# Kernel optimization log

Measured on AMD Instinct MI355X. Metric: run time of the kernel, lower is better.

Reference implementation:

```python
import jax, jax.numpy as jnp
import numpy as np

B, D, H, E, K, A = 65536, 44, 256, 4, 2, 8  # batch, state_dim, hidden, experts, top_k, action_dim


def setup_inputs() -> dict:
    key = jax.random.key(0)
    ks = jax.random.split(key, 10)
    s = 0.1  # weight scale
    return dict(
        state=jax.random.normal(ks[0], (B, D), dtype=jnp.float32),
        rW1=jax.random.normal(ks[1], (D, H // 2)) * s, rb1=jnp.zeros((H // 2,)),
        rW2=jax.random.normal(ks[2], (H // 2, E)) * s, rb2=jnp.zeros((E,)),
        eW1=jax.random.normal(ks[3], (E, D, H)) * s, eb1=jnp.zeros((E, H)),
        eg1=jnp.ones((E, H)), ebt1=jnp.zeros((E, H)),
        eW2=jax.random.normal(ks[4], (E, H, H)) * s, eb2=jnp.zeros((E, H)),
        eg2=jnp.ones((E, H)), ebt2=jnp.zeros((E, H)),
        eW3=jax.random.normal(ks[5], (E, H, 2 * A)) * s, eb3=jnp.zeros((E, 2 * A)),
        vW1=jax.random.normal(ks[6], (D, H)) * s, vb1=jnp.zeros((H,)),
        vg=jnp.ones((H,)), vbt=jnp.zeros((H,)),
        vW2=jax.random.normal(ks[7], (H, H // 2)) * s, vb2=jnp.zeros((H // 2,)),
        vW3=jax.random.normal(ks[8], (H // 2, 1)) * s, vb3=jnp.zeros((1,)),
    )


def _ln(x, g, b):
    m = jnp.mean(x, axis=-1, keepdims=True)
    v = jnp.mean(jnp.square(x - m), axis=-1, keepdims=True)
    return (x - m) * jax.lax.rsqrt(v + 1e-5) * g + b


def reference(state, rW1, rb1, rW2, rb2,
              eW1, eb1, eg1, ebt1, eW2, eb2, eg2, ebt2, eW3, eb3,
              vW1, vb1, vg, vbt, vW2, vb2, vW3, vb3):
    # Router (eval mode: no noise)
    h = jax.nn.relu(state @ rW1 + rb1)
    router_probs = jax.nn.softmax(h @ rW2 + rb2, axis=-1)          # [B, E]
    top_v, top_i = jax.lax.top_k(router_probs, K)                  # [B, K]
    top_v = top_v / (jnp.sum(top_v, axis=-1, keepdims=True) + 1e-8)
    # Dense combine weights per expert (equivalent to per-sample gather/scatter loop)
    combine = jnp.sum(jax.nn.one_hot(top_i, E, dtype=state.dtype) * top_v[..., None], axis=1)  # [B, E]

    def expert(W1, b1, g1, bt1, W2, b2, g2, bt2, W3, b3):
        y = jax.nn.relu(_ln(state @ W1 + b1, g1, bt1))   # [B, H]
        y = jax.nn.relu(_ln(y @ W2 + b2, g2, bt2))       # [B, H]
        return y @ W3 + b3                               # [B, 2A]

    eout = jax.vmap(expert)(eW1, eb1, eg1, ebt1, eW2, eb2, eg2, ebt2, eW3, eb3)  # [E, B, 2A]
    mix = jnp.einsum('ebd,be->bd', eout, combine)        # [B, 2A]

    alpha = jax.nn.softplus(mix[:, :A]) + 1.0
    beta = jax.nn.softplus(mix[:, A:]) + 1.0

    v = jax.nn.relu(_ln(state @ vW1 + vb1, vg, vbt))
    v = jax.nn.relu(v @ vW2 + vb2)
    value = v @ vW3 + vb3                                # [B, 1]
    return alpha, beta, value, router_probs
```

## Files before the change

kernel.cpp:

```cpp
#include <hip/hip_runtime.h>
#include <math.h>

#define NB 65536

using f32x4 = __attribute__((ext_vector_type(4))) float;
using u32x4 = __attribute__((ext_vector_type(4))) unsigned;
using bf16x8 = __attribute__((ext_vector_type(8))) __bf16;

__device__ __forceinline__ unsigned pk2(float lo, float hi) {
    return (unsigned)__builtin_bit_cast(unsigned short, (__bf16)lo)
         | ((unsigned)__builtin_bit_cast(unsigned short, (__bf16)hi) << 16);
}
__device__ __forceinline__ float softplus_f(float x) {
    return fmaxf(x, 0.f) + log1pf(expf(-fabsf(x)));
}

#define MFMA16(acc, a, b) acc = __builtin_amdgcn_mfma_f32_16x16x32_bf16(a, b, acc, 0, 0, 0)

__device__ __forceinline__ bf16x8 cvt8(f32x4 a, f32x4 b) {
    union { bf16x8 v; unsigned u[4]; } r;
    r.u[0] = pk2(a[0], a[1]); r.u[1] = pk2(a[2], a[3]);
    r.u[2] = pk2(b[0], b[1]); r.u[3] = pk2(b[2], b[3]);
    return r.v;
}

__device__ __forceinline__ const bf16x8* ys_frag(const unsigned short* ys, int row, int col) {
    return (const bf16x8*)&ys[row * 256 + (col ^ ((row & 7) << 3))];
}

template<int NJ>
__device__ __forceinline__ void ldch(f32x4* r, const f32x4* __restrict__ src, int tid) {
    #pragma unroll
    for (int j = 0; j < NJ; ++j) r[j] = src[tid + j * 256];
}
template<int NJ>
__device__ __forceinline__ void wrch(unsigned short* buf, const f32x4* r, int tid) {
    #pragma unroll
    for (int j = 0; j < NJ; ++j) *(f32x4*)&buf[(size_t)(tid + j * 256) * 8] = r[j];
}

template<int NT>
__device__ __forceinline__ void mfma_bcols(f32x4* acc, bf16x8 a, const unsigned short* bufp, int c, int g) {
    #pragma unroll
    for (int t = 0; t < NT; ++t) {
        bf16x8 b = *(const bf16x8*)&bufp[t * 512 + g * 128 + c * 8];
        MFMA16(acc[t], a, b);
    }
}

__device__ __forceinline__ void ln_relu_store(
    f32x4* acc, const float* bs, const float* gs, const float* ts,
    unsigned int* ysu, int stripe, int g, int c)
{
    #pragma unroll
    for (int t = 0; t < 16; ++t) {
        float bb = bs[t * 16 + c];
        #pragma unroll
        for (int r = 0; r < 4; ++r) acc[t][r] += bb;
    }
    float sum[4] = {0.f, 0.f, 0.f, 0.f}, sq[4] = {0.f, 0.f, 0.f, 0.f};
    #pragma unroll
    for (int t = 0; t < 16; ++t) {
        #pragma unroll
        for (int r = 0; r < 4; ++r) { sum[r] += acc[t][r]; sq[r] += acc[t][r] * acc[t][r]; }
    }
    #pragma unroll
    for (int m = 1; m < 16; m <<= 1) {
        #pragma unroll
        for (int r = 0; r < 4; ++r) { sum[r] += __shfl_xor(sum[r], m); sq[r] += __shfl_xor(sq[r], m); }
    }
    float rs[4], nm[4];
    #pragma unroll
    for (int r = 0; r < 4; ++r) {
        float mean = sum[r] * (1.f / 256.f);
        float var = sq[r] * (1.f / 256.f) - mean * mean;
        rs[r] = rsqrtf(var + 1e-5f);
        nm[r] = -mean * rs[r];
    }
    const int odd = c & 1;
    const int ra = stripe + g * 4 + (odd ? 2 : 0);
    const int sza = (ra & 7) << 2, szb = ((ra + 1) & 7) << 2;
    #pragma unroll
    for (int t = 0; t < 16; ++t) {
        float gg = gs[t * 16 + c], bb = ts[t * 16 + c];
        float v0 = fmaxf(fmaf(fmaf(acc[t][0], rs[0], nm[0]), gg, bb), 0.f);
        float v1 = fmaxf(fmaf(fmaf(acc[t][1], rs[1], nm[1]), gg, bb), 0.f);
        float v2 = fmaxf(fmaf(fmaf(acc[t][2], rs[2], nm[2]), gg, bb), 0.f);
        float v3 = fmaxf(fmaf(fmaf(acc[t][3], rs[3], nm[3]), gg, bb), 0.f);
        float o0 = __shfl_xor(v0, 1), o1 = __shfl_xor(v1, 1);
        float o2 = __shfl_xor(v2, 1), o3 = __shfl_xor(v3, 1);
        unsigned p0 = pk2(odd ? o0 : v0, odd ? v0 : o0);
        unsigned p1 = pk2(odd ? o1 : v1, odd ? v1 : o1);
        unsigned p2 = pk2(odd ? o2 : v2, odd ? v2 : o2);
        unsigned p3 = pk2(odd ? o3 : v3, odd ? v3 : o3);
        unsigned pa = odd ? p2 : p0;
        unsigned pb = odd ? p3 : p1;
        int cp = t * 8 + (c >> 1);
        ysu[ra * 128 + (cp ^ sza)] = pa;
        ysu[(ra + 1) * 128 + (cp ^ szb)] = pb;
    }
}

__global__ __launch_bounds__(256) void k1_prep_router(
    const float* __restrict__ state,
    const float* __restrict__ rW1, const float* __restrict__ rb1,
    const float* __restrict__ rW2, const float* __restrict__ rb2,
    const float* __restrict__ eW1, const float* __restrict__ eW2, const float* __restrict__ eW3,
    const float* __restrict__ vW1, const float* __restrict__ vW2,
    unsigned int* __restrict__ w1img, unsigned int* __restrict__ w2img,
    unsigned int* __restrict__ vw1img, unsigned int* __restrict__ vw2img,
    unsigned int* __restrict__ w3img,
    float* __restrict__ out_probs, float* __restrict__ combine)
{
    const int blk = blockIdx.x;
    if (blk < 192) {
        int fid = blk * 256 + threadIdx.x;
        float v[8];
        unsigned int* dst;
        if (fid < 8192) {
            int e = fid >> 11, ch = (fid >> 10) & 1, rr = fid & 1023;
            int t = rr >> 6, g = (rr >> 4) & 3, c = rr & 15;
            int h = t * 16 + c, k0 = ch * 32 + g * 8;
            #pragma unroll
            for (int j = 0; j < 8; ++j) {
                int k = k0 + j;
                v[j] = (k < 44) ? eW1[(e * 44 + k) * 256 + h] : 0.f;
            }
            dst = w1img + (size_t)fid * 4;
        } else if (fid < 40960) {
            int f = fid - 8192;
            int e = f >> 13, ch = (f >> 10) & 7, rr = f & 1023;
            int t = rr >> 6, g = (rr >> 4) & 3, c = rr & 15;
            int h = t * 16 + c, k0 = ch * 32 + g * 8;
            const float* base = eW2 + (size_t)e * 65536 + h;
            #pragma unroll
            for (int j = 0; j < 8; ++j) v[j] = base[(size_t)(k0 + j) * 256];
            dst = w2img + (size_t)f * 4;
        } else if (fid < 43008) {
            int f = fid - 40960;
            int ch = f >> 10, rr = f & 1023;
            int t = rr >> 6, g = (rr >> 4) & 3, c = rr & 15;
            int h = t * 16 + c, k0 = ch * 32 + g * 8;
            #pragma unroll
            for (int j = 0; j < 8; ++j) {
                int k = k0 + j;
                v[j] = (k < 44) ? vW1[k * 256 + h] : 0.f;
            }
            dst = vw1img + (size_t)f * 4;
        } else if (fid < 47104) {
            int f = fid - 43008;
            int ch = f >> 9, rr = f & 511;
            int t = rr >> 6, g = (rr >> 4) & 3, c = rr & 15;
            int h = t * 16 + c, k0 = ch * 32 + g * 8;
            #pragma unroll
            for (int j = 0; j < 8; ++j) v[j] = vW2[(k0 + j) * 128 + h];
            dst = vw2img + (size_t)f * 4;
        } else {
            int f = fid - 47104;
            int e = f >> 9, rr = f & 511;
            int s = rr >> 6, g = (rr >> 4) & 3, o = rr & 15;
            int k0 = s * 32 + g * 8;
            #pragma unroll
            for (int j = 0; j < 8; ++j) v[j] = eW3[(size_t)e * 4096 + (k0 + j) * 16 + o];
            dst = w3img + (size_t)f * 4;
        }
        u32x4 out;
        #pragma unroll
        for (int p = 0; p < 4; ++p) out[p] = pk2(v[2 * p], v[2 * p + 1]);
        *(u32x4*)dst = out;
        return;
    }

    int b = (blk - 192) * 256 + threadIdx.x;
    float s[44];
    const float* sp = state + (size_t)b * 44;
    #pragma unroll
    for (int d = 0; d < 44; ++d) s[d] = sp[d];

    float l0 = rb2[0], l1 = rb2[1], l2 = rb2[2], l3 = rb2[3];
    for (int j4 = 0; j4 < 32; ++j4) {
        f32x4 h = *(const f32x4*)&rb1[j4 * 4];
        #pragma unroll
        for (int d = 0; d < 44; ++d) {
            f32x4 w = *(const f32x4*)&rW1[d * 128 + j4 * 4];
            h += s[d] * w;
        }
        #pragma unroll
        for (int jj = 0; jj < 4; ++jj) {
            float hv = fmaxf(h[jj], 0.f);
            f32x4 w2 = *(const f32x4*)&rW2[(j4 * 4 + jj) * 4];
            l0 += hv * w2[0]; l1 += hv * w2[1]; l2 += hv * w2[2]; l3 += hv * w2[3];
        }
    }
    float mx = fmaxf(fmaxf(l0, l1), fmaxf(l2, l3));
    float e0 = expf(l0 - mx), e1 = expf(l1 - mx), e2 = expf(l2 - mx), e3 = expf(l3 - mx);
    float inv = 1.f / (e0 + e1 + e2 + e3);
    float p0 = e0 * inv, p1 = e1 * inv, p2 = e2 * inv, p3 = e3 * inv;
    f32x4 probs = {p0, p1, p2, p3};
    *(f32x4*)&out_probs[(size_t)b * 4] = probs;

    int i1 = 0; float v1 = p0;
    if (p1 > v1) { v1 = p1; i1 = 1; }
    if (p2 > v1) { v1 = p2; i1 = 2; }
    if (p3 > v1) { v1 = p3; i1 = 3; }
    int i2 = -1; float v2 = -1.f;
    if (i1 != 0 && p0 > v2) { v2 = p0; i2 = 0; }
    if (i1 != 1 && p1 > v2) { v2 = p1; i2 = 1; }
    if (i1 != 2 && p2 > v2) { v2 = p2; i2 = 2; }
    if (i1 != 3 && p3 > v2) { v2 = p3; i2 = 3; }
    float cn = 1.f / (v1 + v2 + 1e-8f);
    float c1 = v1 * cn, c2 = v2 * cn;
    f32x4 cm;
    cm[0] = (i1 == 0) ? c1 : (i2 == 0) ? c2 : 0.f;
    cm[1] = (i1 == 1) ? c1 : (i2 == 1) ? c2 : 0.f;
    cm[2] = (i1 == 2) ? c1 : (i2 == 2) ? c2 : 0.f;
    cm[3] = (i1 == 3) ? c1 : (i2 == 3) ? c2 : 0.f;
    *(f32x4*)&combine[(size_t)b * 4] = cm;
}

#define SM_YS    0
#define SM_BUFA  32768
#define SM_BUFB  49152
#define SM_B1    65536
#define SM_G1    66560
#define SM_T1    67584
#define SM_B2    68608
#define SM_G2    69632
#define SM_T2    70656
#define SM_B3    71680
#define SM_CMB   71744
#define SM_TOTAL 72768

#define SWAPBUF() { unsigned short* _t = cur; cur = nxt; nxt = _t; }

__global__ __launch_bounds__(256, 2) void k2_experts_value(
    const float* __restrict__ state,
    const float* __restrict__ eb1, const float* __restrict__ eg1, const float* __restrict__ ebt1,
    const float* __restrict__ eb2, const float* __restrict__ eg2, const float* __restrict__ ebt2,
    const float* __restrict__ eb3,
    const float* __restrict__ vb1, const float* __restrict__ vg, const float* __restrict__ vbt,
    const float* __restrict__ vb2, const float* __restrict__ vW3, const float* __restrict__ vb3,
    const f32x4* __restrict__ w1v, const f32x4* __restrict__ w2v,
    const f32x4* __restrict__ vw1v, const f32x4* __restrict__ vw2v,
    const f32x4* __restrict__ w3v,
    const float* __restrict__ combine,
    float* __restrict__ out_alpha, float* __restrict__ out_beta, float* __restrict__ out_value)
{
    __shared__ __align__(16) unsigned char smem[SM_TOTAL];
    unsigned short* ys = (unsigned short*)(smem + SM_YS);
    unsigned int* ysu = (unsigned int*)(smem + SM_YS);
    float* b1s = (float*)(smem + SM_B1);
    float* g1s = (float*)(smem + SM_G1);
    float* t1s = (float*)(smem + SM_T1);
    float* b2s = (float*)(smem + SM_B2);
    float* g2s = (float*)(smem + SM_G2);
    float* t2s = (float*)(smem + SM_T2);
    float* b3s = (float*)(smem + SM_B3);
    float* cmbs = (float*)(smem + SM_CMB);
    unsigned short* cur = (unsigned short*)(smem + SM_BUFA);
    unsigned short* nxt = (unsigned short*)(smem + SM_BUFB);

    const int tid = threadIdx.x;
    const int wid = tid >> 6;
    const int lane = tid & 63;
    const int c = lane & 15;
    const int g = lane >> 4;
    const int stripe = wid * 16;
    const bool is_expert = (blockIdx.x < 1024);
    const int brow = (is_expert ? blockIdx.x : (blockIdx.x - 1024)) * 64;

    bf16x8 a1[2];
    {
        const float* srow = state + (size_t)(brow + stripe + c) * 44;
        f32x4 v0 = *(const f32x4*)(srow + g * 8);
        f32x4 v1 = *(const f32x4*)(srow + g * 8 + 4);
        a1[0] = cvt8(v0, v1);
        f32x4 z = {0.f, 0.f, 0.f, 0.f};
        f32x4 w0 = z, w1 = z;
        if (g == 0) { w0 = *(const f32x4*)(srow + 32); w1 = *(const f32x4*)(srow + 36); }
        else if (g == 1) { w0 = *(const f32x4*)(srow + 40); }
        a1[1] = cvt8(w0, w1);
    }

    f32x4 r[4];

    if (is_expert) {
        cmbs[tid] = combine[(size_t)brow * 4 + tid];
        float mix0 = 0.f, mix1 = 0.f, mix2 = 0.f, mix3 = 0.f;

        ldch<4>(r, w1v, tid);
        wrch<4>(cur, r, tid);
        ldch<4>(r, w1v + 1024, tid);
        __syncthreads();

        for (int e = 0; e < 4; ++e) {
            const int en = (e < 3) ? e + 1 : 3;
            float xb1 = eb1[e * 256 + tid], xg1 = eg1[e * 256 + tid], xt1 = ebt1[e * 256 + tid];
            float xb2 = eb2[e * 256 + tid], xg2 = eg2[e * 256 + tid], xt2 = ebt2[e * 256 + tid];
            b1s[tid] = xb1; g1s[tid] = xg1; t1s[tid] = xt1;
            b2s[tid] = xb2; g2s[tid] = xg2; t2s[tid] = xt2;
            if (tid < 16) b3s[tid] = eb3[e * 16 + tid];

            f32x4 acc1[16];
            #pragma unroll
            for (int t = 0; t < 16; ++t) acc1[t] = (f32x4){0.f, 0.f, 0.f, 0.f};

            wrch<4>(nxt, r, tid);
            ldch<4>(r, w2v + (size_t)(e * 8 + 0) * 1024, tid);
            mfma_bcols<16>(acc1, a1[0], cur, c, g);
            __syncthreads(); SWAPBUF();

            wrch<4>(nxt, r, tid);
            ldch<4>(r, w2v + (size_t)(e * 8 + 1) * 1024, tid);
            mfma_bcols<16>(acc1, a1[1], cur, c, g);
            ln_relu_store(acc1, b1s, g1s, t1s, ysu, stripe, g, c);
            __syncthreads(); SWAPBUF();

            f32x4 acc2[16];
            #pragma unroll
            for (int t = 0; t < 16; ++t) acc2[t] = (f32x4){0.f, 0.f, 0.f, 0.f};

            #pragma unroll
            for (int ch = 0; ch < 7; ++ch) {
                wrch<4>(nxt, r, tid);
                if (ch < 6) ldch<4>(r, w2v + (size_t)(e * 8 + ch + 2) * 1024, tid);
                else        ldch<2>(r, w3v + (size_t)e * 512, tid);
                bf16x8 a = *ys_frag(ys, stripe + c, ch * 32 + g * 8);
                mfma_bcols<16>(acc2, a, cur, c, g);
                __syncthreads(); SWAPBUF();
            }

            wrch<2>(nxt, r, tid);
            ldch<4>(r, w1v + (size_t)(en * 2) * 1024, tid);
            {
                bf16x8 a = *ys_frag(ys, stripe + c, 7 * 32 + g * 8);
                mfma_bcols<16>(acc2, a, cur, c, g);
            }
            ln_relu_store(acc2, b2s, g2s, t2s, ysu, stripe, g, c);
            __syncthreads(); SWAPBUF();

            wrch<4>(nxt, r, tid);
            ldch<4>(r, w1v + (size_t)(en * 2 + 1) * 1024, tid);
            f32x4 acc3 = (f32x4){0.f, 0.f, 0.f, 0.f};
            #pragma unroll
            for (int s = 0; s < 8; ++s) {
                bf16x8 a = *ys_frag(ys, stripe + c, s * 32 + g * 8);
                bf16x8 b = *(const bf16x8*)&cur[s * 512 + g * 128 + c * 8];
                MFMA16(acc3, a, b);
            }
            float bb3 = b3s[c];
            mix0 += cmbs[(stripe + g * 4 + 0) * 4 + e] * (acc3[0] + bb3);
            mix1 += cmbs[(stripe + g * 4 + 1) * 4 + e] * (acc3[1] + bb3);
            mix2 += cmbs[(stripe + g * 4 + 2) * 4 + e] * (acc3[2] + bb3);
            mix3 += cmbs[(stripe + g * 4 + 3) * 4 + e] * (acc3[3] + bb3);
            __syncthreads(); SWAPBUF();
        }

        int row0 = brow + stripe + g * 4;
        float sp0 = softplus_f(mix0) + 1.f;
        float sp1 = softplus_f(mix1) + 1.f;
        float sp2 = softplus_f(mix2) + 1.f;
        float sp3 = softplus_f(mix3) + 1.f;
        if (c < 8) {
            out_alpha[(size_t)(row0 + 0) * 8 + c] = sp0;
            out_alpha[(size_t)(row0 + 1) * 8 + c] = sp1;
            out_alpha[(size_t)(row0 + 2) * 8 + c] = sp2;
            out_alpha[(size_t)(row0 + 3) * 8 + c] = sp3;
        } else {
            out_beta[(size_t)(row0 + 0) * 8 + (c - 8)] = sp0;
            out_beta[(size_t)(row0 + 1) * 8 + (c - 8)] = sp1;
            out_beta[(size_t)(row0 + 2) * 8 + (c - 8)] = sp2;
            out_beta[(size_t)(row0 + 3) * 8 + (c - 8)] = sp3;
        }
    } else {
        b1s[tid] = vb1[tid]; g1s[tid] = vg[tid]; t1s[tid] = vbt[tid];
        if (tid < 128) { b2s[tid] = vb2[tid]; g2s[tid] = vW3[tid]; }

        ldch<4>(r, vw1v, tid);
        wrch<4>(cur, r, tid);
        ldch<4>(r, vw1v + 1024, tid);
        __syncthreads();

        f32x4 acc1[16];
        #pragma unroll
        for (int t = 0; t < 16; ++t) acc1[t] = (f32x4){0.f, 0.f, 0.f, 0.f};

        wrch<4>(nxt, r, tid);
        ldch<2>(r, vw2v, tid);
        mfma_bcols<16>(acc1, a1[0], cur, c, g);
        __syncthreads(); SWAPBUF();

        wrch<4>(nxt, r, tid);
        ldch<2>(r, vw2v + 512, tid);
        mfma_bcols<16>(acc1, a1[1], cur, c, g);
        ln_relu_store(acc1, b1s, g1s, t1s, ysu, stripe, g, c);
        __syncthreads(); SWAPBUF();

        f32x4 acc2[8];
        #pragma unroll
        for (int t = 0; t < 8; ++t) acc2[t] = (f32x4){0.f, 0.f, 0.f, 0.f};

        #pragma unroll
        for (int ch = 0; ch < 7; ++ch) {
            wrch<2>(nxt, r, tid);
            if (ch < 6) ldch<2>(r, vw2v + (size_t)(ch + 2) * 512, tid);
            bf16x8 a = *ys_frag(ys, stripe + c, ch * 32 + g * 8);
            mfma_bcols<8>(acc2, a, cur, c, g);
            __syncthreads(); SWAPBUF();
        }
        {
            bf16x8 a = *ys_frag(ys, stripe + c, 7 * 32 + g * 8);
            mfma_bcols<8>(acc2, a, cur, c, g);
        }

        float part[4] = {0.f, 0.f, 0.f, 0.f};
        #pragma unroll
        for (int t = 0; t < 8; ++t) {
            float bb = b2s[t * 16 + c], ww = g2s[t * 16 + c];
            #pragma unroll
            for (int q = 0; q < 4; ++q) part[q] += fmaxf(acc2[t][q] + bb, 0.f) * ww;
        }
        #pragma unroll
        for (int m = 1; m < 16; m <<= 1) {
            #pragma unroll
            for (int q = 0; q < 4; ++q) part[q] += __shfl_xor(part[q], m);
        }
        if (c == 0) {
            float v3 = vb3[0];
            int row = brow + stripe + g * 4;
            out_value[row + 0] = part[0] + v3;
            out_value[row + 1] = part[1] + v3;
            out_value[row + 2] = part[2] + v3;
            out_value[row + 3] = part[3] + v3;
        }
    }
}

extern "C" void kernel_launch(void* const* d_in, const int* in_sizes, int n_in,
                              void* d_out, int out_size, void* d_ws, size_t ws_size,
                              hipStream_t stream)
{
    const float* state = (const float*)d_in[0];
    const float* rW1  = (const float*)d_in[1];
    const float* rb1  = (const float*)d_in[2];
    const float* rW2  = (const float*)d_in[3];
    const float* rb2  = (const float*)d_in[4];
    const float* eW1  = (const float*)d_in[5];
    const float* eb1  = (const float*)d_in[6];
    const float* eg1  = (const float*)d_in[7];
    const float* ebt1 = (const float*)d_in[8];
    const float* eW2  = (const float*)d_in[9];
    const float* eb2  = (const float*)d_in[10];
    const float* eg2  = (const float*)d_in[11];
    const float* ebt2 = (const float*)d_in[12];
    const float* eW3  = (const float*)d_in[13];
    const float* eb3  = (const float*)d_in[14];
    const float* vW1  = (const float*)d_in[15];
    const float* vb1  = (const float*)d_in[16];
    const float* vg   = (const float*)d_in[17];
    const float* vbt  = (const float*)d_in[18];
    const float* vW2  = (const float*)d_in[19];
    const float* vb2  = (const float*)d_in[20];
    const float* vW3  = (const float*)d_in[21];
    const float* vb3  = (const float*)d_in[22];

    float* out = (float*)d_out;
    float* out_alpha = out;
    float* out_beta  = out + (size_t)NB * 8;
    float* out_value = out + (size_t)NB * 16;
    float* out_probs = out + (size_t)NB * 17;

    char* ws = (char*)d_ws;
    float* combine        = (float*)ws;
    unsigned int* w1img   = (unsigned int*)(ws + 0x100000);
    unsigned int* w2img   = (unsigned int*)(ws + 0x120000);
    unsigned int* vw1img  = (unsigned int*)(ws + 0x1A0000);
    unsigned int* vw2img  = (unsigned int*)(ws + 0x1A8000);
    unsigned int* w3img   = (unsigned int*)(ws + 0x1B8000);

    hipLaunchKernelGGL(k1_prep_router, dim3(448), dim3(256), 0, stream,
                       state, rW1, rb1, rW2, rb2, eW1, eW2, eW3, vW1, vW2,
                       w1img, w2img, vw1img, vw2img, w3img, out_probs, combine);
    hipLaunchKernelGGL(k2_experts_value, dim3(2048), dim3(256), 0, stream,
                       state, eb1, eg1, ebt1, eb2, eg2, ebt2, eb3,
                       vb1, vg, vbt, vb2, vW3, vb3,
                       (const f32x4*)w1img, (const f32x4*)w2img,
                       (const f32x4*)vw1img, (const f32x4*)vw2img,
                       (const f32x4*)w3img,
                       combine, out_alpha, out_beta, out_value);
}
```

Measured before the change: 279.0 us.

## Fuse router MLP and top-k combine into expert kernel blocks

Moves the router computation (MLP, softmax, top-2 combine weights) from the prep kernel into the expert blocks of the main kernel. Each of the four waves computes a 32-hidden slice of the router for the block's 64 rows, the partial logits are reduced through shared memory, and wave 0 writes the probabilities and combine weights into LDS. This removes the combine-buffer round trip through global memory and shrinks the first kernel to weight repacking only, but it adds scalar FP32 router work and an extra barrier at the start of every expert block.

```diff
diff --git a/kernel.cpp b/kernel.cpp
--- a/kernel.cpp
+++ b/kernel.cpp
@@ -101,121 +101,67 @@
     }
 }
 
-__global__ __launch_bounds__(256) void k1_prep_router(
-    const float* __restrict__ state,
-    const float* __restrict__ rW1, const float* __restrict__ rb1,
-    const float* __restrict__ rW2, const float* __restrict__ rb2,
+__global__ __launch_bounds__(256) void k1_prep(
     const float* __restrict__ eW1, const float* __restrict__ eW2, const float* __restrict__ eW3,
     const float* __restrict__ vW1, const float* __restrict__ vW2,
     unsigned int* __restrict__ w1img, unsigned int* __restrict__ w2img,
     unsigned int* __restrict__ vw1img, unsigned int* __restrict__ vw2img,
-    unsigned int* __restrict__ w3img,
-    float* __restrict__ out_probs, float* __restrict__ combine)
+    unsigned int* __restrict__ w3img)
 {
-    const int blk = blockIdx.x;
-    if (blk < 192) {
-        int fid = blk * 256 + threadIdx.x;
-        float v[8];
-        unsigned int* dst;
-        if (fid < 8192) {
-            int e = fid >> 11, ch = (fid >> 10) & 1, rr = fid & 1023;
-            int t = rr >> 6, g = (rr >> 4) & 3, c = rr & 15;
-            int h = t * 16 + c, k0 = ch * 32 + g * 8;
-            #pragma unroll
-            for (int j = 0; j < 8; ++j) {
-                int k = k0 + j;
-                v[j] = (k < 44) ? eW1[(e * 44 + k) * 256 + h] : 0.f;
-            }
-            dst = w1img + (size_t)fid * 4;
-        } else if (fid < 40960) {
-            int f = fid - 8192;
-            int e = f >> 13, ch = (f >> 10) & 7, rr = f & 1023;
-            int t = rr >> 6, g = (rr >> 4) & 3, c = rr & 15;
-            int h = t * 16 + c, k0 = ch * 32 + g * 8;
-            const float* base = eW2 + (size_t)e * 65536 + h;
-            #pragma unroll
-            for (int j = 0; j < 8; ++j) v[j] = base[(size_t)(k0 + j) * 256];
-            dst = w2img + (size_t)f * 4;
-        } else if (fid < 43008) {
-            int f = fid - 40960;
-            int ch = f >> 10, rr = f & 1023;
-            int t = rr >> 6, g = (rr >> 4) & 3, c = rr & 15;
-            int h = t * 16 + c, k0 = ch * 32 + g * 8;
-            #pragma unroll
-            for (int j = 0; j < 8; ++j) {
-                int k = k0 + j;
-                v[j] = (k < 44) ? vW1[k * 256 + h] : 0.f;
-            }
-            dst = vw1img + (size_t)f * 4;
-        } else if (fid < 47104) {
-            int f = fid - 43008;
-            int ch = f >> 9, rr = f & 511;
-            int t = rr >> 6, g = (rr >> 4) & 3, c = rr & 15;
-            int h = t * 16 + c, k0 = ch * 32 + g * 8;
-            #pragma unroll
-            for (int j = 0; j < 8; ++j) v[j] = vW2[(k0 + j) * 128 + h];
-            dst = vw2img + (size_t)f * 4;
-        } else {
-            int f = fid - 47104;
-            int e = f >> 9, rr = f & 511;
-            int s = rr >> 6, g = (rr >> 4) & 3, o = rr & 15;
-            int k0 = s * 32 + g * 8;
-            #pragma unroll
-            for (int j = 0; j < 8; ++j) v[j] = eW3[(size_t)e * 4096 + (k0 + j) * 16 + o];
-            dst = w3img + (size_t)f * 4;
-        }
-        u32x4 out;
-        #pragma unroll
-        for (int p = 0; p < 4; ++p) out[p] = pk2(v[2 * p], v[2 * p + 1]);
-        *(u32x4*)dst = out;
-        return;
-    }
-
-    int b = (blk - 192) * 256 + threadIdx.x;
-    float s[44];
-    const float* sp = state + (size_t)b * 44;
-    #pragma unroll
-    for (int d = 0; d < 44; ++d) s[d] = sp[d];
-
-    float l0 = rb2[0], l1 = rb2[1], l2 = rb2[2], l3 = rb2[3];
-    for (int j4 = 0; j4 < 32; ++j4) {
-        f32x4 h = *(const f32x4*)&rb1[j4 * 4];
-        #pragma unroll
-        for (int d = 0; d < 44; ++d) {
-            f32x4 w = *(const f32x4*)&rW1[d * 128 + j4 * 4];
-            h += s[d] * w;
-        }
-        #pragma unroll
-        for (int jj = 0; jj < 4; ++jj) {
-            float hv = fmaxf(h[jj], 0.f);
-            f32x4 w2 = *(const f32x4*)&rW2[(j4 * 4 + jj) * 4];
-            l0 += hv * w2[0]; l1 += hv * w2[1]; l2 += hv * w2[2]; l3 += hv * w2[3];
-        }
-    }
-    float mx = fmaxf(fmaxf(l0, l1), fmaxf(l2, l3));
-    float e0 = expf(l0 - mx), e1 = expf(l1 - mx), e2 = expf(l2 - mx), e3 = expf(l3 - mx);
-    float inv = 1.f / (e0 + e1 + e2 + e3);
-    float p0 = e0 * inv, p1 = e1 * inv, p2 = e2 * inv, p3 = e3 * inv;
-    f32x4 probs = {p0, p1, p2, p3};
-    *(f32x4*)&out_probs[(size_t)b * 4] = probs;
-
-    int i1 = 0; float v1 = p0;
-    if (p1 > v1) { v1 = p1; i1 = 1; }
-    if (p2 > v1) { v1 = p2; i1 = 2; }
-    if (p3 > v1) { v1 = p3; i1 = 3; }
-    int i2 = -1; float v2 = -1.f;
-    if (i1 != 0 && p0 > v2) { v2 = p0; i2 = 0; }
-    if (i1 != 1 && p1 > v2) { v2 = p1; i2 = 1; }
-    if (i1 != 2 && p2 > v2) { v2 = p2; i2 = 2; }
-    if (i1 != 3 && p3 > v2) { v2 = p3; i2 = 3; }
-    float cn = 1.f / (v1 + v2 + 1e-8f);
-    float c1 = v1 * cn, c2 = v2 * cn;
-    f32x4 cm;
-    cm[0] = (i1 == 0) ? c1 : (i2 == 0) ? c2 : 0.f;
-    cm[1] = (i1 == 1) ? c1 : (i2 == 1) ? c2 : 0.f;
-    cm[2] = (i1 == 2) ? c1 : (i2 == 2) ? c2 : 0.f;
-    cm[3] = (i1 == 3) ? c1 : (i2 == 3) ? c2 : 0.f;
-    *(f32x4*)&combine[(size_t)b * 4] = cm;
+    int fid = blockIdx.x * 256 + threadIdx.x;
+    float v[8];
+    unsigned int* dst;
+    if (fid < 8192) {
+        int e = fid >> 11, ch = (fid >> 10) & 1, rr = fid & 1023;
+        int t = rr >> 6, g = (rr >> 4) & 3, c = rr & 15;
+        int h = t * 16 + c, k0 = ch * 32 + g * 8;
+        #pragma unroll
+        for (int j = 0; j < 8; ++j) {
+            int k = k0 + j;
+            v[j] = (k < 44) ? eW1[(e * 44 + k) * 256 + h] : 0.f;
+        }
+        dst = w1img + (size_t)fid * 4;
+    } else if (fid < 40960) {
+        int f = fid - 8192;
+        int e = f >> 13, ch = (f >> 10) & 7, rr = f & 1023;
+        int t = rr >> 6, g = (rr >> 4) & 3, c = rr & 15;
+        int h = t * 16 + c, k0 = ch * 32 + g * 8;
+        const float* base = eW2 + (size_t)e * 65536 + h;
+        #pragma unroll
+        for (int j = 0; j < 8; ++j) v[j] = base[(size_t)(k0 + j) * 256];
+        dst = w2img + (size_t)f * 4;
+    } else if (fid < 43008) {
+        int f = fid - 40960;
+        int ch = f >> 10, rr = f & 1023;
+        int t = rr >> 6, g = (rr >> 4) & 3, c = rr & 15;
+        int h = t * 16 + c, k0 = ch * 32 + g * 8;
+        #pragma unroll
+        for (int j = 0; j < 8; ++j) {
+            int k = k0 + j;
+            v[j] = (k < 44) ? vW1[k * 256 + h] : 0.f;
+        }
+        dst = vw1img + (size_t)f * 4;
+    } else if (fid < 47104) {
+        int f = fid - 43008;
+        int ch = f >> 9, rr = f & 511;
+        int t = rr >> 6, g = (rr >> 4) & 3, c = rr & 15;
+        int h = t * 16 + c, k0 = ch * 32 + g * 8;
+        #pragma unroll
+        for (int j = 0; j < 8; ++j) v[j] = vW2[(k0 + j) * 128 + h];
+        dst = vw2img + (size_t)f * 4;
+    } else {
+        int f = fid - 47104;
+        int e = f >> 9, rr = f & 511;
+        int s = rr >> 6, g = (rr >> 4) & 3, o = rr & 15;
+        int k0 = s * 32 + g * 8;
+        #pragma unroll
+        for (int j = 0; j < 8; ++j) v[j] = eW3[(size_t)e * 4096 + (k0 + j) * 16 + o];
+        dst = w3img + (size_t)f * 4;
+    }
+    u32x4 out;
+    #pragma unroll
+    for (int p = 0; p < 4; ++p) out[p] = pk2(v[2 * p], v[2 * p + 1]);
+    *(u32x4*)dst = out;
 }
 
 #define SM_YS    0
@@ -235,6 +181,8 @@
 
 __global__ __launch_bounds__(256, 2) void k2_experts_value(
     const float* __restrict__ state,
+    const float* __restrict__ rW1, const float* __restrict__ rb1,
+    const float* __restrict__ rW2, const float* __restrict__ rb2,
     const float* __restrict__ eb1, const float* __restrict__ eg1, const float* __restrict__ ebt1,
     const float* __restrict__ eb2, const float* __restrict__ eg2, const float* __restrict__ ebt2,
     const float* __restrict__ eb3,
@@ -243,8 +191,8 @@
     const f32x4* __restrict__ w1v, const f32x4* __restrict__ w2v,
     const f32x4* __restrict__ vw1v, const f32x4* __restrict__ vw2v,
     const f32x4* __restrict__ w3v,
-    const float* __restrict__ combine,
-    float* __restrict__ out_alpha, float* __restrict__ out_beta, float* __restrict__ out_value)
+    float* __restrict__ out_alpha, float* __restrict__ out_beta, float* __restrict__ out_value,
+    float* __restrict__ out_probs)
 {
     __shared__ __align__(16) unsigned char smem[SM_TOTAL];
     unsigned short* ys = (unsigned short*)(smem + SM_YS);
@@ -285,13 +233,78 @@
     f32x4 r[4];
 
     if (is_expert) {
-        cmbs[tid] = combine[(size_t)brow * 4 + tid];
-        float mix0 = 0.f, mix1 = 0.f, mix2 = 0.f, mix3 = 0.f;
-
         ldch<4>(r, w1v, tid);
+
+        const int widu = __builtin_amdgcn_readfirstlane(wid);
+        f32x4* pl = (f32x4*)(smem + SM_BUFB);
+        {
+            float s[44];
+            {
+                const float* srow2 = state + (size_t)(brow + lane) * 44;
+                #pragma unroll
+                for (int d4 = 0; d4 < 11; ++d4) {
+                    f32x4 v = *(const f32x4*)(srow2 + d4 * 4);
+                    s[d4 * 4 + 0] = v[0]; s[d4 * 4 + 1] = v[1];
+                    s[d4 * 4 + 2] = v[2]; s[d4 * 4 + 3] = v[3];
+                }
+            }
+            const float* w1b = rW1 + widu * 32;
+            f32x4 h[8];
+            #pragma unroll
+            for (int j = 0; j < 8; ++j) h[j] = *(const f32x4*)&rb1[widu * 32 + j * 4];
+            #pragma unroll
+            for (int d = 0; d < 44; ++d) {
+                #pragma unroll
+                for (int j = 0; j < 8; ++j)
+                    h[j] += s[d] * *(const f32x4*)(w1b + d * 128 + j * 4);
+            }
+            f32x4 l = {0.f, 0.f, 0.f, 0.f};
+            #pragma unroll
+            for (int j = 0; j < 8; ++j) {
+                #pragma unroll
+                for (int cmp = 0; cmp < 4; ++cmp) {
+                    float hv = fmaxf(h[j][cmp], 0.f);
+                    l += hv * *(const f32x4*)&rW2[(widu * 32 + j * 4 + cmp) * 4];
+                }
+            }
+            pl[widu * 64 + lane] = l;
+        }
+        __syncthreads();
+        if (wid == 0) {
+            f32x4 lg = pl[lane] + pl[64 + lane] + pl[128 + lane] + pl[192 + lane];
+            lg += *(const f32x4*)rb2;
+            float l0 = lg[0], l1 = lg[1], l2 = lg[2], l3 = lg[3];
+            float mx = fmaxf(fmaxf(l0, l1), fmaxf(l2, l3));
+            float e0 = expf(l0 - mx), e1 = expf(l1 - mx), e2 = expf(l2 - mx), e3 = expf(l3 - mx);
+            float inv = 1.f / (e0 + e1 + e2 + e3);
+            float p0 = e0 * inv, p1 = e1 * inv, p2 = e2 * inv, p3 = e3 * inv;
+            f32x4 probs = {p0, p1, p2, p3};
+            *(f32x4*)&out_probs[(size_t)(brow + lane) * 4] = probs;
+
+            int i1 = 0; float v1 = p0;
+            if (p1 > v1) { v1 = p1; i1 = 1; }
+            if (p2 > v1) { v1 = p2; i1 = 2; }
+            if (p3 > v1) { v1 = p3; i1 = 3; }
+            int i2 = -1; float v2 = -1.f;
+            if (i1 != 0 && p0 > v2) { v2 = p0; i2 = 0; }
+            if (i1 != 1 && p1 > v2) { v2 = p1; i2 = 1; }
+            if (i1 != 2 && p2 > v2) { v2 = p2; i2 = 2; }
+            if (i1 != 3 && p3 > v2) { v2 = p3; i2 = 3; }
+            float cn = 1.f / (v1 + v2 + 1e-8f);
+            float c1 = v1 * cn, c2 = v2 * cn;
+            f32x4 cm;
+            cm[0] = (i1 == 0) ? c1 : (i2 == 0) ? c2 : 0.f;
+            cm[1] = (i1 == 1) ? c1 : (i2 == 1) ? c2 : 0.f;
+            cm[2] = (i1 == 2) ? c1 : (i2 == 2) ? c2 : 0.f;
+            cm[3] = (i1 == 3) ? c1 : (i2 == 3) ? c2 : 0.f;
+            *(f32x4*)&cmbs[lane * 4] = cm;
+        }
+
         wrch<4>(cur, r, tid);
         ldch<4>(r, w1v + 1024, tid);
         __syncthreads();
+
+        float mix0 = 0.f, mix1 = 0.f, mix2 = 0.f, mix3 = 0.f;
 
         for (int e = 0; e < 4; ++e) {
             const int en = (e < 3) ? e + 1 : 3;
@@ -471,21 +484,21 @@
     float* out_probs = out + (size_t)NB * 17;
 
     char* ws = (char*)d_ws;
-    float* combine        = (float*)ws;
-    unsigned int* w1img   = (unsigned int*)(ws + 0x100000);
-    unsigned int* w2img   = (unsigned int*)(ws + 0x120000);
-    unsigned int* vw1img  = (unsigned int*)(ws + 0x1A0000);
-    unsigned int* vw2img  = (unsigned int*)(ws + 0x1A8000);
-    unsigned int* w3img   = (unsigned int*)(ws + 0x1B8000);
-
-    hipLaunchKernelGGL(k1_prep_router, dim3(448), dim3(256), 0, stream,
-                       state, rW1, rb1, rW2, rb2, eW1, eW2, eW3, vW1, vW2,
-                       w1img, w2img, vw1img, vw2img, w3img, out_probs, combine);
+    unsigned int* w1img   = (unsigned int*)(ws + 0x00000);
+    unsigned int* w2img   = (unsigned int*)(ws + 0x20000);
+    unsigned int* vw1img  = (unsigned int*)(ws + 0xA0000);
+    unsigned int* vw2img  = (unsigned int*)(ws + 0xA8000);
+    unsigned int* w3img   = (unsigned int*)(ws + 0xB8000);
+
+    hipLaunchKernelGGL(k1_prep, dim3(192), dim3(256), 0, stream,
+                       eW1, eW2, eW3, vW1, vW2,
+                       w1img, w2img, vw1img, vw2img, w3img);
     hipLaunchKernelGGL(k2_experts_value, dim3(2048), dim3(256), 0, stream,
-                       state, eb1, eg1, ebt1, eb2, eg2, ebt2, eb3,
+                       state, rW1, rb1, rW2, rb2,
+                       eb1, eg1, ebt1, eb2, eg2, ebt2, eb3,
                        vb1, vg, vbt, vb2, vW3, vb3,
                        (const f32x4*)w1img, (const f32x4*)w2img,
                        (const f32x4*)vw1img, (const f32x4*)vw2img,
                        (const f32x4*)w3img,
-                       combine, out_alpha, out_beta, out_value);
-}
+                       out_alpha, out_beta, out_value, out_probs);
+}
```

After: 263.0 us. -5.7%, faster.

## Split router hidden dimension across waves with shared-memory logit reduction

Applied to the files above, without the earlier changes.

The router stage now assigns 64 batch rows per block and splits the 128 hidden units across four waves, each wave computing partial logits that are summed through shared memory before softmax and top-2. This quadruples the number of router blocks to raise occupancy and makes weight addresses wave-uniform for scalar loads. It adds a block barrier and shared-memory traffic, and leaves three waves idle during the softmax/top-k tail.

```diff
diff --git a/kernel.cpp b/kernel.cpp
--- a/kernel.cpp
+++ b/kernel.cpp
@@ -112,6 +112,7 @@
     unsigned int* __restrict__ w3img,
     float* __restrict__ out_probs, float* __restrict__ combine)
 {
+    __shared__ f32x4 pl[256];
     const int blk = blockIdx.x;
     if (blk < 192) {
         int fid = blk * 256 + threadIdx.x;
@@ -171,51 +172,72 @@
         return;
     }
 
-    int b = (blk - 192) * 256 + threadIdx.x;
-    float s[44];
-    const float* sp = state + (size_t)b * 44;
-    #pragma unroll
-    for (int d = 0; d < 44; ++d) s[d] = sp[d];
-
-    float l0 = rb2[0], l1 = rb2[1], l2 = rb2[2], l3 = rb2[3];
-    for (int j4 = 0; j4 < 32; ++j4) {
-        f32x4 h = *(const f32x4*)&rb1[j4 * 4];
+    const int tid = threadIdx.x;
+    const int wid = tid >> 6;
+    const int lane = tid & 63;
+    const int brow = (blk - 192) * 64;
+    const int w32 = __builtin_amdgcn_readfirstlane(wid * 32);
+
+    {
+        float s[44];
+        const float* srow = state + (size_t)(brow + lane) * 44;
+        #pragma unroll
+        for (int d4 = 0; d4 < 11; ++d4) {
+            f32x4 v = *(const f32x4*)(srow + d4 * 4);
+            s[d4 * 4 + 0] = v[0]; s[d4 * 4 + 1] = v[1];
+            s[d4 * 4 + 2] = v[2]; s[d4 * 4 + 3] = v[3];
+        }
+        const float* w1b = rW1 + w32;
+        f32x4 h[8];
+        #pragma unroll
+        for (int j = 0; j < 8; ++j) h[j] = *(const f32x4*)&rb1[w32 + j * 4];
         #pragma unroll
         for (int d = 0; d < 44; ++d) {
-            f32x4 w = *(const f32x4*)&rW1[d * 128 + j4 * 4];
-            h += s[d] * w;
-        }
-        #pragma unroll
-        for (int jj = 0; jj < 4; ++jj) {
-            float hv = fmaxf(h[jj], 0.f);
-            f32x4 w2 = *(const f32x4*)&rW2[(j4 * 4 + jj) * 4];
-            l0 += hv * w2[0]; l1 += hv * w2[1]; l2 += hv * w2[2]; l3 += hv * w2[3];
-        }
-    }
-    float mx = fmaxf(fmaxf(l0, l1), fmaxf(l2, l3));
-    float e0 = expf(l0 - mx), e1 = expf(l1 - mx), e2 = expf(l2 - mx), e3 = expf(l3 - mx);
-    float inv = 1.f / (e0 + e1 + e2 + e3);
-    float p0 = e0 * inv, p1 = e1 * inv, p2 = e2 * inv, p3 = e3 * inv;
-    f32x4 probs = {p0, p1, p2, p3};
-    *(f32x4*)&out_probs[(size_t)b * 4] = probs;
-
-    int i1 = 0; float v1 = p0;
-    if (p1 > v1) { v1 = p1; i1 = 1; }
-    if (p2 > v1) { v1 = p2; i1 = 2; }
-    if (p3 > v1) { v1 = p3; i1 = 3; }
-    int i2 = -1; float v2 = -1.f;
-    if (i1 != 0 && p0 > v2) { v2 = p0; i2 = 0; }
-    if (i1 != 1 && p1 > v2) { v2 = p1; i2 = 1; }
-    if (i1 != 2 && p2 > v2) { v2 = p2; i2 = 2; }
-    if (i1 != 3 && p3 > v2) { v2 = p3; i2 = 3; }
-    float cn = 1.f / (v1 + v2 + 1e-8f);
-    float c1 = v1 * cn, c2 = v2 * cn;
-    f32x4 cm;
-    cm[0] = (i1 == 0) ? c1 : (i2 == 0) ? c2 : 0.f;
-    cm[1] = (i1 == 1) ? c1 : (i2 == 1) ? c2 : 0.f;
-    cm[2] = (i1 == 2) ? c1 : (i2 == 2) ? c2 : 0.f;
-    cm[3] = (i1 == 3) ? c1 : (i2 == 3) ? c2 : 0.f;
-    *(f32x4*)&combine[(size_t)b * 4] = cm;
+            #pragma unroll
+            for (int j = 0; j < 8; ++j)
+                h[j] += s[d] * *(const f32x4*)(w1b + d * 128 + j * 4);
+        }
+        f32x4 l = {0.f, 0.f, 0.f, 0.f};
+        #pragma unroll
+        for (int j = 0; j < 8; ++j) {
+            #pragma unroll
+            for (int cmp = 0; cmp < 4; ++cmp) {
+                float hv = fmaxf(h[j][cmp], 0.f);
+                l += hv * *(const f32x4*)&rW2[(w32 + j * 4 + cmp) * 4];
+            }
+        }
+        pl[wid * 64 + lane] = l;
+    }
+    __syncthreads();
+    if (wid == 0) {
+        f32x4 lg = pl[lane] + pl[64 + lane] + pl[128 + lane] + pl[192 + lane];
+        lg += *(const f32x4*)rb2;
+        float l0 = lg[0], l1 = lg[1], l2 = lg[2], l3 = lg[3];
+        float mx = fmaxf(fmaxf(l0, l1), fmaxf(l2, l3));
+        float e0 = expf(l0 - mx), e1 = expf(l1 - mx), e2 = expf(l2 - mx), e3 = expf(l3 - mx);
+        float inv = 1.f / (e0 + e1 + e2 + e3);
+        float p0 = e0 * inv, p1 = e1 * inv, p2 = e2 * inv, p3 = e3 * inv;
+        f32x4 probs = {p0, p1, p2, p3};
+        *(f32x4*)&out_probs[(size_t)(brow + lane) * 4] = probs;
+
+        int i1 = 0; float v1 = p0;
+        if (p1 > v1) { v1 = p1; i1 = 1; }
+        if (p2 > v1) { v1 = p2; i1 = 2; }
+        if (p3 > v1) { v1 = p3; i1 = 3; }
+        int i2 = -1; float v2 = -1.f;
+        if (i1 != 0 && p0 > v2) { v2 = p0; i2 = 0; }
+        if (i1 != 1 && p1 > v2) { v2 = p1; i2 = 1; }
+        if (i1 != 2 && p2 > v2) { v2 = p2; i2 = 2; }
+        if (i1 != 3 && p3 > v2) { v2 = p3; i2 = 3; }
+        float cn = 1.f / (v1 + v2 + 1e-8f);
+        float c1 = v1 * cn, c2 = v2 * cn;
+        f32x4 cm;
+        cm[0] = (i1 == 0) ? c1 : (i2 == 0) ? c2 : 0.f;
+        cm[1] = (i1 == 1) ? c1 : (i2 == 1) ? c2 : 0.f;
+        cm[2] = (i1 == 2) ? c1 : (i2 == 2) ? c2 : 0.f;
+        cm[3] = (i1 == 3) ? c1 : (i2 == 3) ? c2 : 0.f;
+        *(f32x4*)&combine[(size_t)(brow + lane) * 4] = cm;
+    }
 }
 
 #define SM_YS    0
@@ -478,7 +500,7 @@
     unsigned int* vw2img  = (unsigned int*)(ws + 0x1A8000);
     unsigned int* w3img   = (unsigned int*)(ws + 0x1B8000);
 
-    hipLaunchKernelGGL(k1_prep_router, dim3(448), dim3(256), 0, stream,
+    hipLaunchKernelGGL(k1_prep_router, dim3(1216), dim3(256), 0, stream,
                        state, rW1, rb1, rW2, rb2, eW1, eW2, eW3, vW1, vW2,
                        w1img, w2img, vw1img, vw2img, w3img, out_probs, combine);
     hipLaunchKernelGGL(k2_experts_value, dim3(2048), dim3(256), 0, stream,
```

Result: faster. 259.2 us (-7.1%).
